# Kernel tuning notes

Measured on AMD Instinct MI355X. Metric: run time of the kernel, lower is better.

## Reference

```python
import jax, jax.numpy as jnp
import numpy as np

HIDDEN = 2048
NUM_OPS = 3
BATCH = 16384


def setup_inputs() -> dict:
    key = jax.random.key(0)
    ks = jax.random.split(key, 6)
    x = jax.random.normal(ks[0], (BATCH, HIDDEN), dtype=jnp.float32)
    chosen_ops = jax.random.randint(ks[1], (BATCH,), 0, NUM_OPS, dtype=jnp.int32)
    # Stacked expert params; torch nn.Linear computes x @ W.T + b, W: [out, in].
    # We store W already transposed to [in, out] for direct einsum.
    scale = 1.0 / np.sqrt(HIDDEN)
    W1 = jax.random.uniform(ks[2], (NUM_OPS, HIDDEN, HIDDEN), jnp.float32, -scale, scale)
    b1 = jax.random.uniform(ks[3], (NUM_OPS, HIDDEN), jnp.float32, -scale, scale)
    W2 = jax.random.uniform(ks[4], (NUM_OPS, HIDDEN, HIDDEN), jnp.float32, -scale, scale)
    b2 = jax.random.uniform(ks[5], (NUM_OPS, HIDDEN), jnp.float32, -scale, scale)
    return {"x": x, "W1": W1, "b1": b1, "W2": W2, "b2": b2, "chosen_ops": chosen_ops}


def reference(x, W1, b1, W2, b2, chosen_ops):
    # Temper.apply_operators: each row of x is routed to one expert MLP:
    #   out[i] = relu(W2_e @ relu(W1_e @ x[i] + b1_e) + b2_e), e = chosen_ops[i]
    # operator_freshness starts at zeros, so the +0.01*result branch is inactive.
    # Vectorized: run all experts on all rows (small fixed NUM_OPS), then select.
    h = jax.nn.relu(jnp.einsum('bh,ehk->ebk', x, W1) + b1[:, None, :])   # [E,B,H]
    y = jax.nn.relu(jnp.einsum('ebh,ehk->ebk', h, W2) + b2[:, None, :])  # [E,B,H]
    out = y[chosen_ops, jnp.arange(x.shape[0]), :]                        # [B,H]
    return out
```

## Files before the change

### kernel.cpp

```cpp
#include <hip/hip_runtime.h>
#include <hip/hip_bf16.h>
#include <stdint.h>

#define HIDDEN 2048
#define BATCH 16384
#define NUM_OPS 3
#define NTILES 131
#define M_CAP (NTILES * 128)
#define NXT 16

typedef __attribute__((ext_vector_type(4))) float f32x4;
typedef __attribute__((ext_vector_type(8))) short short8;
typedef __attribute__((ext_vector_type(8))) __bf16 bf16x8;

static constexpr size_t XB_SZ   = (size_t)M_CAP * HIDDEN * 2;
static constexpr size_t H_SZ    = XB_SZ;
static constexpr size_t WT_SZ   = (size_t)NUM_OPS * HIDDEN * HIDDEN * 2;
static constexpr size_t PERM_SZ = (size_t)M_CAP * 4;

__device__ __forceinline__ unsigned f2bf(float f) {
  unsigned u = __float_as_uint(f);
  return (u + 0x7FFFu + ((u >> 16) & 1u)) >> 16;
}

__device__ __forceinline__ void async_ld16(const void* g, void* l) {
  __builtin_amdgcn_global_load_lds(
      (__attribute__((address_space(1))) void*)(void*)g,
      (__attribute__((address_space(3))) void*)l, 16, 0, 0);
}

__global__ __launch_bounds__(256) void k_count(const int* __restrict__ ops,
                                               int* __restrict__ cnt,
                                               int* __restrict__ perm) {
  int i = blockIdx.x * 256 + threadIdx.x;
  if (i < M_CAP) perm[i] = -1;
  int e = (i < BATCH) ? ops[i] : -1;
  int lane = threadIdx.x & 63;
#pragma unroll
  for (int ee = 0; ee < NUM_OPS; ee++) {
    unsigned long long m = __ballot(e == ee);
    if (lane == 0 && m) atomicAdd(&cnt[ee], __popcll(m));
  }
}

__global__ void k_scan(const int* __restrict__ cnt, int* __restrict__ seg,
                       int* __restrict__ te) {
  int a0 = (cnt[0] + 127) & ~127;
  int a1 = (cnt[1] + 127) & ~127;
  int a2 = (cnt[2] + 127) & ~127;
  if (threadIdx.x == 0) {
    seg[0] = 0; seg[1] = a0; seg[2] = a0 + a1; seg[3] = a0 + a1 + a2;
  }
  for (int t = threadIdx.x; t < NTILES; t += 64) {
    int row = t * 128;
    int ex = -1;
    if (row < a0) ex = 0;
    else if (row < a0 + a1) ex = 1;
    else if (row < a0 + a1 + a2) ex = 2;
    te[t] = ex;
  }
}

__global__ __launch_bounds__(256) void k_perm(const int* __restrict__ ops,
                                              const int* __restrict__ seg,
                                              int* __restrict__ c2,
                                              int* __restrict__ perm) {
  int b = blockIdx.x * 256 + threadIdx.x;
  int e = (b < BATCH) ? ops[b] : -1;
  int lane = threadIdx.x & 63;
#pragma unroll
  for (int ee = 0; ee < NUM_OPS; ee++) {
    unsigned long long m = __ballot(e == ee);
    if (m) {
      int base = 0;
      if (lane == 0) base = atomicAdd(&c2[ee], __popcll(m));
      base = __shfl(base, 0);
      if (e == ee) {
        int myoff = __popcll(m & ((1ull << lane) - 1ull));
        perm[seg[ee] + base + myoff] = b;
      }
    }
  }
}

__global__ __launch_bounds__(256) void k_prep(const float* __restrict__ x,
                                              const int* __restrict__ perm,
                                              short* __restrict__ xb,
                                              const float* __restrict__ W1,
                                              const float* __restrict__ W2,
                                              short* __restrict__ W1t,
                                              short* __restrict__ W2t) {
  int tid = threadIdx.x;
  if (blockIdx.x < M_CAP) {
    int pos = blockIdx.x;
    int b = perm[pos];
    uint4 o;
    if (b < 0) {
      o = make_uint4(0u, 0u, 0u, 0u);
    } else {
      const float4* xs = (const float4*)(x + (size_t)b * HIDDEN + tid * 8);
      float4 f0 = xs[0], f1 = xs[1];
      o.x = f2bf(f0.x) | (f2bf(f0.y) << 16);
      o.y = f2bf(f0.z) | (f2bf(f0.w) << 16);
      o.z = f2bf(f1.x) | (f2bf(f1.y) << 16);
      o.w = f2bf(f1.z) | (f2bf(f1.w) << 16);
    }
    *(uint4*)(xb + (size_t)pos * HIDDEN + tid * 8) = o;
  } else {
    __shared__ float t[64][65];
    int q = blockIdx.x - M_CAP;
    int z = q >> 10;
    int rem = q & 1023;
    int by = rem >> 5, bx = rem & 31;
    const float* src = (z < 3) ? (W1 + (size_t)z * HIDDEN * HIDDEN)
                               : (W2 + (size_t)(z - 3) * HIDDEN * HIDDEN);
    short* dst = (z < 3) ? (W1t + (size_t)z * HIDDEN * HIDDEN)
                         : (W2t + (size_t)(z - 3) * HIDDEN * HIDDEN);
    int k0 = by * 64;
    int n0 = bx * 64;
    {
      int kk = tid >> 4, n4 = (tid & 15) * 4;
#pragma unroll
      for (int p = 0; p < 4; p++) {
        int k = p * 16 + kk;
        *(float4*)&t[k][n4] = *(const float4*)&src[(size_t)(k0 + k) * HIDDEN + n0 + n4];
      }
    }
    __syncthreads();
#pragma unroll
    for (int p = 0; p < 2; p++) {
      int qq = p * 256 + tid;
      int n = qq >> 3, uc = qq & 7;
      uint4 o;
      unsigned* po = (unsigned*)&o;
#pragma unroll
      for (int j = 0; j < 4; j++) {
        float a = t[uc * 8 + 2 * j][n];
        float c = t[uc * 8 + 2 * j + 1][n];
        po[j] = f2bf(a) | (f2bf(c) << 16);
      }
      *(uint4*)&dst[(size_t)(n0 + n) * HIDDEN + k0 + uc * 8] = o;
    }
  }
}

template <int SECOND>
__global__ __launch_bounds__(256)
void gemm_fused(const short* __restrict__ A, const short* __restrict__ Wt,
                const float* __restrict__ bias, const int* __restrict__ te,
                const int* __restrict__ perm, short* __restrict__ Hout,
                float* __restrict__ Yout) {
  __shared__ short As[128 * 64];
  __shared__ short Bs[128 * 64];

  const int lin = blockIdx.x;
  const int slot = lin >> 3;
  const int yt = slot >> 1;
  const int xt = (lin & 7) + 8 * (slot & 1);

  const int e = te[yt];
  if (e < 0) return;

  const int tid = threadIdx.x;
  const int wave = tid >> 6;
  const int lane = tid & 63;
  const int quad = lane >> 4;
  const int l16 = lane & 15;
  const int wm = (wave >> 1) * 64;
  const int wn = (wave & 1) * 64;

  const short* Ag = A + (size_t)yt * 128 * HIDDEN;
  const short* Bg = Wt + (size_t)e * HIDDEN * HIDDEN + (size_t)xt * 128 * HIDDEN;

  const int crow = tid >> 3;
  const int csw = ((tid & 7) ^ (crow & 7)) * 8;

  f32x4 acc[4][4] = {};

  for (int k0 = 0; k0 < HIDDEN; k0 += 64) {
#pragma unroll
    for (int i = 0; i < 4; i++)
      async_ld16(Ag + (size_t)(i * 32 + crow) * HIDDEN + (k0 + csw),
                 As + (i * 256 + wave * 64) * 8);
#pragma unroll
    for (int i = 0; i < 4; i++)
      async_ld16(Bg + (size_t)(i * 32 + crow) * HIDDEN + (k0 + csw),
                 Bs + (i * 256 + wave * 64) * 8);
    __syncthreads();
#pragma unroll
    for (int kk = 0; kk < 64; kk += 32) {
      bf16x8 af[4], bfr[4];
#pragma unroll
      for (int i = 0; i < 4; i++) {
        int row = wm + i * 16 + l16;
        int col = ((kk >> 3) + quad) ^ (row & 7);
        short8 s = *(const short8*)(As + row * 64 + col * 8);
        af[i] = __builtin_bit_cast(bf16x8, s);
      }
#pragma unroll
      for (int j = 0; j < 4; j++) {
        int row = wn + j * 16 + l16;
        int col = ((kk >> 3) + quad) ^ (row & 7);
        short8 s = *(const short8*)(Bs + row * 64 + col * 8);
        bfr[j] = __builtin_bit_cast(bf16x8, s);
      }
#pragma unroll
      for (int i = 0; i < 4; i++)
#pragma unroll
        for (int j = 0; j < 4; j++)
          acc[i][j] = __builtin_amdgcn_mfma_f32_16x16x32_bf16(af[i], bfr[j], acc[i][j], 0, 0, 0);
    }
    __syncthreads();
  }

  const int rowbase = yt * 128 + wm + quad * 4;
  const int colbase = xt * 128 + wn + l16;
#pragma unroll
  for (int j = 0; j < 4; j++) {
    const int n = colbase + j * 16;
    const float bv = bias[e * HIDDEN + n];
#pragma unroll
    for (int i = 0; i < 4; i++) {
      const int m0 = rowbase + i * 16;
#pragma unroll
      for (int r = 0; r < 4; r++) {
        float v = acc[i][j][r] + bv;
        v = v > 0.0f ? v : 0.0f;
        const int m = m0 + r;
        if (SECOND) {
          const int b = perm[m];
          if (b >= 0) Yout[(size_t)b * HIDDEN + n] = v;
        } else {
          Hout[(size_t)m * HIDDEN + n] = (short)f2bf(v);
        }
      }
    }
  }
}

extern "C" void kernel_launch(void* const* d_in, const int* in_sizes, int n_in,
                              void* d_out, int out_size, void* d_ws, size_t ws_size,
                              hipStream_t stream) {
  const float* x  = (const float*)d_in[0];
  const float* W1 = (const float*)d_in[1];
  const float* b1 = (const float*)d_in[2];
  const float* W2 = (const float*)d_in[3];
  const float* b2 = (const float*)d_in[4];
  const int* ops  = (const int*)d_in[5];
  float* out = (float*)d_out;

  char* ws = (char*)d_ws;
  short* xb  = (short*)(ws);
  short* h   = (short*)(ws + XB_SZ);
  short* w1t = (short*)(ws + XB_SZ + H_SZ);
  short* w2t = (short*)(ws + XB_SZ + H_SZ + WT_SZ);
  int* perm  = (int*)(ws + XB_SZ + H_SZ + 2 * WT_SZ);
  int* meta  = (int*)(ws + XB_SZ + H_SZ + 2 * WT_SZ + PERM_SZ);
  int* cnt = meta;
  int* c2  = meta + 4;
  int* seg = meta + 8;
  int* te  = meta + 16;

  hipMemsetAsync(meta, 0, 32, stream);
  k_count<<<(M_CAP + 255) / 256, 256, 0, stream>>>(ops, cnt, perm);
  k_scan<<<1, 64, 0, stream>>>(cnt, seg, te);
  k_perm<<<BATCH / 256, 256, 0, stream>>>(ops, seg, c2, perm);
  k_prep<<<M_CAP + 6 * 32 * 32, 256, 0, stream>>>(x, perm, xb, W1, W2, w1t, w2t);
  gemm_fused<0><<<NXT * NTILES, 256, 0, stream>>>(xb, w1t, b1, te, perm, h, nullptr);
  gemm_fused<1><<<NXT * NTILES, 256, 0, stream>>>(h, w2t, b2, te, perm, nullptr, out);
}
```

Measured before the change: 721.4 us.

## Rewrite grouped GEMM as 256x256-tile, 8-wave, double-buffered pipelined kernel

Replaces the 128x128, 4-wave GEMM with a 256x256 tile computed by 8 waves (512 threads). It uses 128 KB of dynamic LDS split into two buffers, so global-to-LDS async loads for the next K-step run while MFMAs work on the current one. The K loop is split into four phases with sched_barrier, s_setprio and explicit waitcnt to interleave LDS reads, async loads and matrix ops. Expert segments are now padded to 256 rows, which adds more wasted padding rows. The larger tiles aim to raise arithmetic intensity and hide load latency, at the cost of fewer, larger blocks, higher register pressure and only one block per CU because of the LDS use.

```diff
diff --git a/kernel.cpp b/kernel.cpp
--- a/kernel.cpp
+++ b/kernel.cpp
@@ -5,9 +5,10 @@
 #define HIDDEN 2048
 #define BATCH 16384
 #define NUM_OPS 3
-#define NTILES 131
-#define M_CAP (NTILES * 128)
-#define NXT 16
+#define NT_M 67
+#define M_CAP (NT_M * 256)
+#define NXT 8
+#define KT 32
 
 typedef __attribute__((ext_vector_type(4))) float f32x4;
 typedef __attribute__((ext_vector_type(8))) short short8;
@@ -45,14 +46,14 @@
 
 __global__ void k_scan(const int* __restrict__ cnt, int* __restrict__ seg,
                        int* __restrict__ te) {
-  int a0 = (cnt[0] + 127) & ~127;
-  int a1 = (cnt[1] + 127) & ~127;
-  int a2 = (cnt[2] + 127) & ~127;
+  int a0 = (cnt[0] + 255) & ~255;
+  int a1 = (cnt[1] + 255) & ~255;
+  int a2 = (cnt[2] + 255) & ~255;
   if (threadIdx.x == 0) {
     seg[0] = 0; seg[1] = a0; seg[2] = a0 + a1; seg[3] = a0 + a1 + a2;
   }
-  for (int t = threadIdx.x; t < NTILES; t += 64) {
-    int row = t * 128;
+  for (int t = threadIdx.x; t < NT_M; t += 64) {
+    int row = t * 256;
     int ex = -1;
     if (row < a0) ex = 0;
     else if (row < a0 + a1) ex = 1;
@@ -145,91 +146,171 @@
 }
 
 template <int SECOND>
-__global__ __launch_bounds__(256)
-void gemm_fused(const short* __restrict__ A, const short* __restrict__ Wt,
-                const float* __restrict__ bias, const int* __restrict__ te,
-                const int* __restrict__ perm, short* __restrict__ Hout,
-                float* __restrict__ Yout) {
-  __shared__ short As[128 * 64];
-  __shared__ short Bs[128 * 64];
+__global__ __launch_bounds__(512, 2)
+void gemm256(const short* __restrict__ A, const short* __restrict__ Wt,
+             const float* __restrict__ bias, const int* __restrict__ te,
+             const int* __restrict__ perm, short* __restrict__ Hout,
+             float* __restrict__ Yout) {
+  extern __shared__ short lds[];
 
   const int lin = blockIdx.x;
-  const int slot = lin >> 3;
-  const int yt = slot >> 1;
-  const int xt = (lin & 7) + 8 * (slot & 1);
-
+  const int xt = lin & 7;
+  const int yt = lin >> 3;
   const int e = te[yt];
   if (e < 0) return;
 
   const int tid = threadIdx.x;
-  const int wave = tid >> 6;
+  const int wid = tid >> 6;
   const int lane = tid & 63;
   const int quad = lane >> 4;
   const int l16 = lane & 15;
-  const int wm = (wave >> 1) * 64;
-  const int wn = (wave & 1) * 64;
-
-  const short* Ag = A + (size_t)yt * 128 * HIDDEN;
-  const short* Bg = Wt + (size_t)e * HIDDEN * HIDDEN + (size_t)xt * 128 * HIDDEN;
-
-  const int crow = tid >> 3;
-  const int csw = ((tid & 7) ^ (crow & 7)) * 8;
-
-  f32x4 acc[4][4] = {};
-
-  for (int k0 = 0; k0 < HIDDEN; k0 += 64) {
-#pragma unroll
-    for (int i = 0; i < 4; i++)
-      async_ld16(Ag + (size_t)(i * 32 + crow) * HIDDEN + (k0 + csw),
-                 As + (i * 256 + wave * 64) * 8);
-#pragma unroll
-    for (int i = 0; i < 4; i++)
-      async_ld16(Bg + (size_t)(i * 32 + crow) * HIDDEN + (k0 + csw),
-                 Bs + (i * 256 + wave * 64) * 8);
-    __syncthreads();
-#pragma unroll
-    for (int kk = 0; kk < 64; kk += 32) {
-      bf16x8 af[4], bfr[4];
-#pragma unroll
-      for (int i = 0; i < 4; i++) {
-        int row = wm + i * 16 + l16;
-        int col = ((kk >> 3) + quad) ^ (row & 7);
-        short8 s = *(const short8*)(As + row * 64 + col * 8);
-        af[i] = __builtin_bit_cast(bf16x8, s);
-      }
-#pragma unroll
-      for (int j = 0; j < 4; j++) {
-        int row = wn + j * 16 + l16;
-        int col = ((kk >> 3) + quad) ^ (row & 7);
-        short8 s = *(const short8*)(Bs + row * 64 + col * 8);
-        bfr[j] = __builtin_bit_cast(bf16x8, s);
-      }
-#pragma unroll
-      for (int i = 0; i < 4; i++)
-#pragma unroll
-        for (int j = 0; j < 4; j++)
-          acc[i][j] = __builtin_amdgcn_mfma_f32_16x16x32_bf16(af[i], bfr[j], acc[i][j], 0, 0, 0);
-    }
-    __syncthreads();
-  }
-
-  const int rowbase = yt * 128 + wm + quad * 4;
-  const int colbase = xt * 128 + wn + l16;
-#pragma unroll
-  for (int j = 0; j < 4; j++) {
-    const int n = colbase + j * 16;
-    const float bv = bias[e * HIDDEN + n];
-#pragma unroll
-    for (int i = 0; i < 4; i++) {
-      const int m0 = rowbase + i * 16;
-#pragma unroll
-      for (int r = 0; r < 4; r++) {
-        float v = acc[i][j][r] + bv;
+  const int wmh = wid >> 2;
+  const int wnq = wid & 3;
+  const int brow0 = (wnq & 1) * 64;
+
+  const short* Ag = A + (size_t)yt * 256 * HIDDEN;
+  const short* Bg = Wt + (size_t)e * HIDDEN * HIDDEN + (size_t)xt * 256 * HIDDEN;
+
+  const int r0 = tid >> 3;
+  const int c0 = ((tid & 7) ^ (r0 & 7)) * 8;
+  const short* pA = Ag + (size_t)r0 * HIDDEN + c0;
+  const short* pB = Bg + (size_t)r0 * HIDDEN + c0;
+  const int dstw = wid * 512;
+
+  auto stage = [&](const short* src, int dst) {
+    async_ld16(src, lds + dst + dstw);
+    async_ld16(src + 64 * HIDDEN, lds + dst + 4096 + dstw);
+  };
+  auto frag = [&](int base, int r, int q) {
+    return __builtin_bit_cast(bf16x8,
+        *(const short8*)(lds + base + r * 64 + ((q ^ (r & 7)) * 8)));
+  };
+
+  f32x4 acc[8][4] = {};
+  bf16x8 af[4][2], bA[2][2], bB[2][2];
+
+  stage(pA, 0);
+  stage(pA + 128 * HIDDEN, 8192);
+  stage(pB, 16384);
+  stage(pB + 128 * HIDDEN, 24576);
+  stage(pB + 64, 32768 + 16384);
+  stage(pB + 64 + 128 * HIDDEN, 32768 + 24576);
+  asm volatile("s_waitcnt vmcnt(4)" ::: "memory");
+  __builtin_amdgcn_s_barrier();
+
+  for (int t = 0; t < KT; ++t) {
+    const int b = (t & 1) << 15;
+    const int nb = 32768 - b;
+    const int aMy = b + wmh * 8192;
+    const int bMy = b + 16384 + (wnq >> 1) * 8192;
+    const short* pAn = pA + (t + 1) * 64;
+    const short* pBn = pB + (t + 2) * 64;
+
+#pragma unroll
+    for (int i = 0; i < 4; ++i)
+#pragma unroll
+      for (int s = 0; s < 2; ++s)
+        af[i][s] = frag(aMy, i * 16 + l16, s * 4 + quad);
+#pragma unroll
+    for (int j = 0; j < 2; ++j)
+#pragma unroll
+      for (int s = 0; s < 2; ++s)
+        bA[j][s] = frag(bMy, brow0 + j * 16 + l16, s * 4 + quad);
+    if (t + 1 < KT) stage(pAn, nb);
+    __builtin_amdgcn_sched_barrier(0);
+    __builtin_amdgcn_s_barrier();
+    asm volatile("s_waitcnt lgkmcnt(0)" ::: "memory");
+    __builtin_amdgcn_sched_barrier(0);
+    __builtin_amdgcn_s_setprio(1);
+#pragma unroll
+    for (int i = 0; i < 4; ++i)
+#pragma unroll
+      for (int j = 0; j < 2; ++j)
+#pragma unroll
+        for (int s = 0; s < 2; ++s)
+          acc[i][j] = __builtin_amdgcn_mfma_f32_16x16x32_bf16(af[i][s], bA[j][s], acc[i][j], 0, 0, 0);
+    __builtin_amdgcn_s_setprio(0);
+    __builtin_amdgcn_sched_barrier(0);
+    __builtin_amdgcn_s_barrier();
+
+#pragma unroll
+    for (int j = 0; j < 2; ++j)
+#pragma unroll
+      for (int s = 0; s < 2; ++s)
+        bB[j][s] = frag(bMy, brow0 + 32 + j * 16 + l16, s * 4 + quad);
+    if (t + 1 < KT) stage(pAn + 128 * HIDDEN, nb + 8192);
+    __builtin_amdgcn_sched_barrier(0);
+    __builtin_amdgcn_s_barrier();
+    asm volatile("s_waitcnt lgkmcnt(0)" ::: "memory");
+    __builtin_amdgcn_sched_barrier(0);
+    __builtin_amdgcn_s_setprio(1);
+#pragma unroll
+    for (int i = 0; i < 4; ++i)
+#pragma unroll
+      for (int j = 0; j < 2; ++j)
+#pragma unroll
+        for (int s = 0; s < 2; ++s)
+          acc[i][2 + j] = __builtin_amdgcn_mfma_f32_16x16x32_bf16(af[i][s], bB[j][s], acc[i][2 + j], 0, 0, 0);
+    __builtin_amdgcn_s_setprio(0);
+    __builtin_amdgcn_sched_barrier(0);
+    __builtin_amdgcn_s_barrier();
+
+#pragma unroll
+    for (int i = 0; i < 4; ++i)
+#pragma unroll
+      for (int s = 0; s < 2; ++s)
+        af[i][s] = frag(aMy, 64 + i * 16 + l16, s * 4 + quad);
+    if (t + 2 < KT) stage(pBn, b + 16384);
+    __builtin_amdgcn_sched_barrier(0);
+    __builtin_amdgcn_s_barrier();
+    asm volatile("s_waitcnt lgkmcnt(0)" ::: "memory");
+    __builtin_amdgcn_sched_barrier(0);
+    __builtin_amdgcn_s_setprio(1);
+#pragma unroll
+    for (int i = 0; i < 4; ++i)
+#pragma unroll
+      for (int j = 0; j < 2; ++j)
+#pragma unroll
+        for (int s = 0; s < 2; ++s)
+          acc[4 + i][2 + j] = __builtin_amdgcn_mfma_f32_16x16x32_bf16(af[i][s], bB[j][s], acc[4 + i][2 + j], 0, 0, 0);
+    __builtin_amdgcn_s_setprio(0);
+    __builtin_amdgcn_sched_barrier(0);
+    __builtin_amdgcn_s_barrier();
+
+    if (t + 2 < KT) stage(pBn + 128 * HIDDEN, b + 24576);
+    __builtin_amdgcn_sched_barrier(0);
+    __builtin_amdgcn_s_barrier();
+    __builtin_amdgcn_s_setprio(1);
+#pragma unroll
+    for (int i = 0; i < 4; ++i)
+#pragma unroll
+      for (int j = 0; j < 2; ++j)
+#pragma unroll
+        for (int s = 0; s < 2; ++s)
+          acc[4 + i][j] = __builtin_amdgcn_mfma_f32_16x16x32_bf16(af[i][s], bA[j][s], acc[4 + i][j], 0, 0, 0);
+    __builtin_amdgcn_s_setprio(0);
+    __builtin_amdgcn_sched_barrier(0);
+    if (t + 2 < KT) asm volatile("s_waitcnt vmcnt(4)" ::: "memory");
+    else            asm volatile("s_waitcnt vmcnt(0)" ::: "memory");
+    __builtin_amdgcn_s_barrier();
+  }
+
+  const int rb = yt * 256 + wmh * 128 + quad * 4;
+  const int cb = xt * 256 + wnq * 64 + l16;
+#pragma unroll
+  for (int i = 0; i < 8; ++i) {
+#pragma unroll
+    for (int r = 0; r < 4; ++r) {
+      const int m = rb + i * 16 + r;
+      int bidx = 0;
+      if (SECOND) bidx = perm[m];
+#pragma unroll
+      for (int j = 0; j < 4; ++j) {
+        const int n = cb + j * 16;
+        float v = acc[i][j][r] + bias[e * HIDDEN + n];
         v = v > 0.0f ? v : 0.0f;
-        const int m = m0 + r;
         if (SECOND) {
-          const int b = perm[m];
-          if (b >= 0) Yout[(size_t)b * HIDDEN + n] = v;
+          if (bidx >= 0) Yout[(size_t)bidx * HIDDEN + n] = v;
         } else {
           Hout[(size_t)m * HIDDEN + n] = (short)f2bf(v);
         }
@@ -261,11 +342,20 @@
   int* seg = meta + 8;
   int* te  = meta + 16;
 
+  static bool attr_done = false;
+  if (!attr_done) {
+    hipFuncSetAttribute((const void*)gemm256<0>,
+                        hipFuncAttributeMaxDynamicSharedMemorySize, 131072);
+    hipFuncSetAttribute((const void*)gemm256<1>,
+                        hipFuncAttributeMaxDynamicSharedMemorySize, 131072);
+    attr_done = true;
+  }
+
   hipMemsetAsync(meta, 0, 32, stream);
   k_count<<<(M_CAP + 255) / 256, 256, 0, stream>>>(ops, cnt, perm);
   k_scan<<<1, 64, 0, stream>>>(cnt, seg, te);
   k_perm<<<BATCH / 256, 256, 0, stream>>>(ops, seg, c2, perm);
   k_prep<<<M_CAP + 6 * 32 * 32, 256, 0, stream>>>(x, perm, xb, W1, W2, w1t, w2t);
-  gemm_fused<0><<<NXT * NTILES, 256, 0, stream>>>(xb, w1t, b1, te, perm, h, nullptr);
-  gemm_fused<1><<<NXT * NTILES, 256, 0, stream>>>(h, w2t, b2, te, perm, nullptr, out);
-}
+  gemm256<0><<<NXT * NT_M, 512, 131072, stream>>>(xb, w1t, b1, te, perm, h, nullptr);
+  gemm256<1><<<NXT * NT_M, 512, 131072, stream>>>(h, w2t, b2, te, perm, nullptr, out);
+}
```

Result: faster. 675.3 us (-6.4%).
